# Kernel optimization log

Hardware: AMD Instinct MI355X
Metric: run time of the kernel (lower is better)

The kernel has to match this reference:

```python
import jax, jax.numpy as jnp
import numpy as np

PATCH_LEN = 16
PATCH_STRIDE = 8
DIM = 512
NUM_HEADS = 8
HEAD_DIM = DIM // NUM_HEADS
NUM_LAYERS = 4
MLP_HIDDEN = 4 * DIM
ROPE_BASE = 10000.0
LN_EPS = 1e-5


def setup_inputs() -> dict:
    key = jax.random.key(0)
    ks = jax.random.split(key, 20)
    B, T, C = 4, 8192, 7
    s = 0.02
    inp = {
        "x": jax.random.normal(ks[0], (B, T, C), dtype=jnp.float32),
        "W_emb": jax.random.normal(ks[1], (PATCH_LEN * C, DIM), dtype=jnp.float32) * s,
        "b_emb": jnp.zeros((DIM,), jnp.float32),
        "ln1_g": jnp.ones((NUM_LAYERS, DIM), jnp.float32),
        "ln1_b": jnp.zeros((NUM_LAYERS, DIM), jnp.float32),
        "W_qkv": jax.random.normal(ks[2], (NUM_LAYERS, DIM, 3 * DIM), dtype=jnp.float32) * s,
        "b_qkv": jnp.zeros((NUM_LAYERS, 3 * DIM), jnp.float32),
        "W_proj": jax.random.normal(ks[3], (NUM_LAYERS, DIM, DIM), dtype=jnp.float32) * s,
        "b_proj": jnp.zeros((NUM_LAYERS, DIM), jnp.float32),
        "ln2_g": jnp.ones((NUM_LAYERS, DIM), jnp.float32),
        "ln2_b": jnp.zeros((NUM_LAYERS, DIM), jnp.float32),
        "W_mlp1": jax.random.normal(ks[4], (NUM_LAYERS, DIM, MLP_HIDDEN), dtype=jnp.float32) * s,
        "b_mlp1": jnp.zeros((NUM_LAYERS, MLP_HIDDEN), jnp.float32),
        "W_mlp2": jax.random.normal(ks[5], (NUM_LAYERS, MLP_HIDDEN, DIM), dtype=jnp.float32) * s,
        "b_mlp2": jnp.zeros((NUM_LAYERS, DIM), jnp.float32),
        "lnf_g": jnp.ones((DIM,), jnp.float32),
        "lnf_b": jnp.zeros((DIM,), jnp.float32),
    }
    return inp


def _layer_norm(x, g, b):
    mu = jnp.mean(x, axis=-1, keepdims=True)
    var = jnp.mean(jnp.square(x - mu), axis=-1, keepdims=True)
    return (x - mu) * jax.lax.rsqrt(var + LN_EPS) * g + b


def _rotate_half(x):
    x1, x2 = jnp.split(x, 2, axis=-1)
    return jnp.concatenate((-x2, x1), axis=-1)


def _rope_cos_sin(seq_len):
    t = jnp.arange(seq_len, dtype=jnp.float32)
    inv_freq = 1.0 / (ROPE_BASE ** (jnp.arange(0, HEAD_DIM, 2, dtype=jnp.float32) / HEAD_DIM))
    freqs = jnp.outer(t, inv_freq)                      # [L, hd/2]
    emb = jnp.concatenate((freqs, freqs), axis=-1)      # [L, hd]
    return jnp.cos(emb), jnp.sin(emb)


def _forward(x, W_emb, b_emb, ln1_g, ln1_b, W_qkv, b_qkv, W_proj, b_proj,
             ln2_g, ln2_b, W_mlp1, b_mlp1, W_mlp2, b_mlp2, lnf_g, lnf_b):
    B, T, C = x.shape
    n = (T - PATCH_LEN) // PATCH_STRIDE + 1
    # torch unfold: [B, n, C, patch_len], then flattened as (C, patch_len)
    idx = jnp.arange(n)[:, None] * PATCH_STRIDE + jnp.arange(PATCH_LEN)[None, :]  # [n, P]
    patches = x[:, idx, :]                              # [B, n, P, C]
    patches = patches.transpose(0, 1, 3, 2).reshape(B, n, C * PATCH_LEN)
    emb = patches @ W_emb + b_emb                       # [B, n, D]

    cos, sin = _rope_cos_sin(n)                         # [n, hd]
    cos = cos[None, None, :, :]
    sin = sin[None, None, :, :]
    scale = HEAD_DIM ** -0.5

    h = emb
    for i in range(NUM_LAYERS):
        # --- attention ---
        y = _layer_norm(h, ln1_g[i], ln1_b[i])
        qkv = (y @ W_qkv[i] + b_qkv[i]).reshape(B, n, 3, NUM_HEADS, HEAD_DIM)
        qkv = qkv.transpose(2, 0, 3, 1, 4)              # [3, B, H, n, hd]
        q, k, v = qkv[0], qkv[1], qkv[2]
        q = q * cos + _rotate_half(q) * sin
        k = k * cos + _rotate_half(k) * sin
        attn = jax.nn.softmax(jnp.einsum('bhqd,bhkd->bhqk', q, k) * scale, axis=-1)
        o = jnp.einsum('bhqk,bhkd->bhqd', attn, v)      # [B, H, n, hd]
        o = o.transpose(0, 2, 1, 3).reshape(B, n, DIM)
        h = h + (o @ W_proj[i] + b_proj[i])
        # --- mlp ---
        y = _layer_norm(h, ln2_g[i], ln2_b[i])
        y = jax.nn.gelu(y @ W_mlp1[i] + b_mlp1[i], approximate=False)
        h = h + (y @ W_mlp2[i] + b_mlp2[i])

    x_out = _layer_norm(h, lnf_g, lnf_b)
    return emb, x_out


def reference(x, W_emb, b_emb, ln1_g, ln1_b, W_qkv, b_qkv, W_proj, b_proj,
              ln2_g, ln2_b, W_mlp1, b_mlp1, W_mlp2, b_mlp2, lnf_g, lnf_b):
    return _forward(x, W_emb, b_emb, ln1_g, ln1_b, W_qkv, b_qkv, W_proj, b_proj,
                    ln2_g, ln2_b, W_mlp1, b_mlp1, W_mlp2, b_mlp2, lnf_g, lnf_b)
```

## Files before the change

kernel.cpp:

```cpp
#include <hip/hip_runtime.h>
#include <hip/hip_bf16.h>
#include <math.h>

#define B_SZ 4
#define T_LEN 8192
#define C_IN 7
#define NPATCH 1023
#define DIM 512
#define NH 8
#define HD 64
#define NLAYERS 4
#define MLP_HID 2048
#define M_ROWS (B_SZ * NPATCH)
#define KEMB 128
#define LN_EPS 1e-5f

typedef __attribute__((ext_vector_type(8))) short short8;
typedef __attribute__((ext_vector_type(4))) float float4v;

static __device__ __forceinline__ unsigned short f2bf(float f) {
  __hip_bfloat16 h = __float2bfloat16(f);
  return *reinterpret_cast<unsigned short*>(&h);
}
static __device__ __forceinline__ float bf2f(unsigned short u) {
  return __uint_as_float(((unsigned)u) << 16);
}

__global__ __launch_bounds__(256) void patch_kernel(
    const float* __restrict__ x, unsigned short* __restrict__ Pm) {
  int idx = blockIdx.x * 256 + threadIdx.x;
  if (idx >= M_ROWS * KEMB) return;
  int row = idx >> 7, c = idx & 127;
  float v = 0.f;
  if (c < 112) {
    int b = row / NPATCH, i = row - b * NPATCH;
    int ci = c >> 4, p = c & 15;
    v = x[((size_t)b * T_LEN + (size_t)i * 8 + p) * C_IN + ci];
  }
  Pm[idx] = f2bf(v);
}

__global__ __launch_bounds__(256) void wemb_cvt_kernel(
    const float* __restrict__ W, unsigned short* __restrict__ Wt) {
  int idx = blockIdx.x * 256 + threadIdx.x;
  if (idx >= DIM * KEMB) return;
  int n = idx >> 7, k = idx & 127;
  float v = (k < 112) ? W[(size_t)k * DIM + n] : 0.f;
  Wt[idx] = f2bf(v);
}

template <bool BF>
__global__ __launch_bounds__(256) void ln_kernel(
    const float* __restrict__ in, const float* __restrict__ g,
    const float* __restrict__ bb, void* __restrict__ outv, int M) {
  int row = blockIdx.x * 4 + (threadIdx.x >> 6);
  if (row >= M) return;
  int lane = threadIdx.x & 63;
  const float* xr = in + (size_t)row * DIM;
  float v[8];
  float s = 0.f;
  #pragma unroll
  for (int k = 0; k < 8; ++k) { v[k] = xr[lane + 64 * k]; s += v[k]; }
  #pragma unroll
  for (int off = 32; off; off >>= 1) s += __shfl_down(s, off);
  s = __shfl(s, 0);
  float mu = s * (1.f / DIM);
  float q = 0.f;
  #pragma unroll
  for (int k = 0; k < 8; ++k) { float d = v[k] - mu; q = fmaf(d, d, q); }
  #pragma unroll
  for (int off = 32; off; off >>= 1) q += __shfl_down(q, off);
  q = __shfl(q, 0);
  float rstd = rsqrtf(q * (1.f / DIM) + LN_EPS);
  #pragma unroll
  for (int k = 0; k < 8; ++k) {
    int d = lane + 64 * k;
    float r = (v[k] - mu) * rstd * g[d] + bb[d];
    if (BF)
      ((unsigned short*)outv)[(size_t)row * DIM + d] = f2bf(r);
    else
      ((float*)outv)[(size_t)row * DIM + d] = r;
  }
}

__global__ __launch_bounds__(256) void wcvt_kernel(
    const float* __restrict__ W, unsigned short* __restrict__ Wt, int K, int N) {
  __shared__ float tile[32][33];
  int n0 = blockIdx.x * 32, k0 = blockIdx.y * 32, L = blockIdx.z;
  const float* Ws = W + (size_t)L * K * N;
  unsigned short* Wd = Wt + (size_t)L * K * N;
  int tx = threadIdx.x & 31, ty = threadIdx.x >> 5;
  #pragma unroll
  for (int i = 0; i < 4; ++i)
    tile[ty + i * 8][tx] = Ws[(size_t)(k0 + ty + i * 8) * N + n0 + tx];
  __syncthreads();
  #pragma unroll
  for (int i = 0; i < 4; ++i)
    Wd[(size_t)(n0 + ty + i * 8) * K + k0 + tx] = f2bf(tile[tx][ty + i * 8]);
}

__global__ __launch_bounds__(256) void rope_tab_kernel(float2* __restrict__ tab) {
  int idx = blockIdx.x * 256 + threadIdx.x;
  if (idx >= NPATCH * 32) return;
  int i = idx >> 5, j = idx & 31;
  float inv = powf(10000.0f, -(float)j * (1.0f / 32.0f));
  float sn, cs;
  sincosf((float)i * inv, &sn, &cs);
  tab[idx] = make_float2(cs, sn);
}

template <int TM, int TN, int EPI>
__global__ __launch_bounds__(256) void mfma_gemm(
    const unsigned short* __restrict__ A, const unsigned short* __restrict__ Bt,
    const float* __restrict__ bias, const float* __restrict__ res,
    float* __restrict__ Cf, float* __restrict__ Cf2,
    unsigned short* __restrict__ Cb, const float2* __restrict__ rtab,
    int M, int N, int K) {
  constexpr int WM = TM / 2, WN = TN / 2;
  constexpr int NI = WM / 16, NJ = WN / 16;
  constexpr int ACH = TM * 4;
  constexpr int TCH = (TM + TN) * 4;
  constexpr int CH = TCH / 256;
  __shared__ __align__(16) unsigned short As[2][TM][40];
  __shared__ __align__(16) unsigned short Bs[2][TN][40];
  const int bm = blockIdx.y * TM;
  const int bn = blockIdx.x * TN;
  const int tid = threadIdx.x;
  const int lane = tid & 63, wave = tid >> 6;
  const int quad = lane >> 4, l16 = lane & 15;
  const int wm = (wave & 1) * WM;
  const int wn = (wave >> 1) * WN;

  float4v acc[NI][NJ];
  #pragma unroll
  for (int i = 0; i < NI; ++i)
    #pragma unroll
    for (int j = 0; j < NJ; ++j)
      acc[i][j] = (float4v){0.f, 0.f, 0.f, 0.f};

  uint4 pr[CH];
  auto load_regs = [&](int kk) {
    #pragma unroll
    for (int it = 0; it < CH; ++it) {
      int c = tid + it * 256;
      if (c < ACH) {
        int row = c >> 2, ch = (c & 3) * 8;
        int gm = bm + row;
        pr[it] = make_uint4(0u, 0u, 0u, 0u);
        if (gm < M) pr[it] = *(const uint4*)(A + (size_t)gm * K + kk + ch);
      } else {
        int c2 = c - ACH;
        int row = c2 >> 2, ch = (c2 & 3) * 8;
        pr[it] = *(const uint4*)(Bt + (size_t)(bn + row) * K + kk + ch);
      }
    }
  };

  load_regs(0);
  int buf = 0;
  for (int k0 = 0; k0 < K; k0 += 32, buf ^= 1) {
    #pragma unroll
    for (int it = 0; it < CH; ++it) {
      int c = tid + it * 256;
      if (c < ACH)
        *(uint4*)&As[buf][c >> 2][(c & 3) * 8] = pr[it];
      else {
        int c2 = c - ACH;
        *(uint4*)&Bs[buf][c2 >> 2][(c2 & 3) * 8] = pr[it];
      }
    }
    if (k0 + 32 < K) load_regs(k0 + 32);
    __syncthreads();
    short8 af[NI], bfr[NJ];
    #pragma unroll
    for (int i = 0; i < NI; ++i)
      af[i] = *(const short8*)&As[buf][wm + i * 16 + l16][quad * 8];
    #pragma unroll
    for (int j = 0; j < NJ; ++j)
      bfr[j] = *(const short8*)&Bs[buf][wn + j * 16 + l16][quad * 8];
    #pragma unroll
    for (int i = 0; i < NI; ++i)
      #pragma unroll
      for (int j = 0; j < NJ; ++j)
        acc[i][j] = __builtin_amdgcn_mfma_f32_16x16x32_bf16(
            af[i], bfr[j], acc[i][j], 0, 0, 0);
  }

  if (EPI == 6) {
    const int sec = (bn + wn) >> 9;
    #pragma unroll
    for (int i = 0; i < NI; ++i) {
      int gm0 = bm + wm + i * 16 + quad * 4;
      #pragma unroll
      for (int r = 0; r < 4; ++r) {
        int gm = gm0 + r;
        if (gm >= M) continue;
        size_t rowoff = (size_t)gm * N;
        if (sec < 2) {
          int ip = gm; if (ip >= 2046) ip -= 2046; if (ip >= 1023) ip -= 1023;
          float sc = (sec == 0) ? 0.125f : 1.f;
          #pragma unroll
          for (int j = 0; j < 2; ++j) {
            int gn = bn + wn + j * 16 + l16;
            float v0 = acc[i][j][r] + bias[gn];
            float v1 = acc[i][j + 2][r] + bias[gn + 32];
            float2 t = rtab[ip * 32 + j * 16 + l16];
            Cb[rowoff + gn]      = f2bf((v0 * t.x - v1 * t.y) * sc);
            Cb[rowoff + gn + 32] = f2bf((v1 * t.x + v0 * t.y) * sc);
          }
        } else {
          #pragma unroll
          for (int j = 0; j < 4; ++j) {
            int gn = bn + wn + j * 16 + l16;
            Cb[rowoff + gn] = f2bf(acc[i][j][r] + bias[gn]);
          }
        }
      }
    }
    return;
  }

  #pragma unroll
  for (int j = 0; j < NJ; ++j) {
    int gn = bn + wn + j * 16 + l16;
    float bv = bias[gn];
    #pragma unroll
    for (int i = 0; i < NI; ++i) {
      int gm0 = bm + wm + i * 16 + quad * 4;
      #pragma unroll
      for (int r = 0; r < 4; ++r) {
        int gm = gm0 + r;
        if (gm < M) {
          float v = acc[i][j][r] + bv;
          size_t off = (size_t)gm * N + gn;
          if (EPI == 1) {
            Cf[off] = v + res[off];
          } else if (EPI == 2) {
            Cb[off] = f2bf(0.5f * v * (1.f + erff(v * 0.70710678118f)));
          } else if (EPI == 3) {
            Cb[off] = f2bf(v);
          } else {
            Cf[off] = v;
            Cf2[off] = v;
          }
        }
      }
    }
  }
}

#define APITCH 72

__global__ __launch_bounds__(256) void attn_kernel(
    const unsigned short* __restrict__ qkvb, unsigned short* __restrict__ o) {
  const int qt0 = blockIdx.x * 64;
  const int h = blockIdx.y;
  const int b = blockIdx.z;
  const int tid = threadIdx.x;
  const int lane = tid & 63, wave = tid >> 6;
  const int quad = lane >> 4, l16 = lane & 15;

  __shared__ __align__(16) unsigned short Qs[64][APITCH];
  __shared__ __align__(16) unsigned short Vt[2][HD][APITCH];
  __shared__ __align__(16) unsigned short Ps[4][16][APITCH];

  const int sr = tid >> 2;
  const int sc0 = (tid & 3) * 16;
  {
    int qi = qt0 + sr;
    uint4 a = make_uint4(0u, 0u, 0u, 0u), b2 = a;
    if (qi < NPATCH) {
      const uint4* src = (const uint4*)(qkvb + (size_t)(b * NPATCH + qi) * (3 * DIM) + h * HD + sc0);
      a = src[0]; b2 = src[1];
    }
    *(uint4*)&Qs[sr][sc0] = a;
    *(uint4*)&Qs[sr][sc0 + 8] = b2;
  }

  const int kp = tid & 31, dg = tid >> 5;
  uint4 pv0, pv1;
  auto load_v = [&](int j0) {
    pv0 = pv1 = make_uint4(0u, 0u, 0u, 0u);
    int j = j0 + 2 * kp;
    const unsigned short* vb = qkvb + (size_t)(b * NPATCH + j) * (3 * DIM) + 2 * DIM + h * HD + dg * 8;
    if (j < NPATCH)     pv0 = *(const uint4*)vb;
    if (j + 1 < NPATCH) pv1 = *(const uint4*)(vb + 3 * DIM);
  };

  const unsigned short* kbase = qkvb + (size_t)b * NPATCH * (3 * DIM) + DIM + (size_t)h * HD;
  uint4 nk0[4], nk1[4];
  auto load_k = [&](int j0) {
    #pragma unroll
    for (int j = 0; j < 4; ++j) {
      int row = j0 + j * 16 + l16;
      nk0[j] = make_uint4(0u, 0u, 0u, 0u);
      nk1[j] = nk0[j];
      if (row < NPATCH) {
        const uint4* kr = (const uint4*)(kbase + (size_t)row * (3 * DIM) + quad * 8);
        nk0[j] = kr[0];
        nk1[j] = kr[4];
      }
    }
  };

  load_v(0);
  load_k(0);
  __syncthreads();

  short8 aq0 = *(const short8*)&Qs[wave * 16 + l16][quad * 8];
  short8 aq1 = *(const short8*)&Qs[wave * 16 + l16][32 + quad * 8];

  float4v accO[4];
  #pragma unroll
  for (int j2 = 0; j2 < 4; ++j2) accO[j2] = (float4v){0.f, 0.f, 0.f, 0.f};
  float m_run[4] = {-1e30f, -1e30f, -1e30f, -1e30f};
  float lp[4] = {0.f, 0.f, 0.f, 0.f};

  int buf = 0;
  for (int j0 = 0; j0 < NPATCH; j0 += 64, buf ^= 1) {
    {
      unsigned short va[8], vb8[8];
      *(uint4*)&va[0] = pv0;
      *(uint4*)&vb8[0] = pv1;
      #pragma unroll
      for (int u = 0; u < 8; ++u) {
        unsigned pk = (unsigned)va[u] | ((unsigned)vb8[u] << 16);
        *(unsigned*)&Vt[buf][dg * 8 + u][2 * kp] = pk;
      }
    }
    __syncthreads();

    float4v s[4];
    __builtin_amdgcn_s_setprio(1);
    #pragma unroll
    for (int j = 0; j < 4; ++j) {
      s[j] = (float4v){0.f, 0.f, 0.f, 0.f};
      s[j] = __builtin_amdgcn_mfma_f32_16x16x32_bf16(
          aq0, __builtin_bit_cast(short8, nk0[j]), s[j], 0, 0, 0);
      s[j] = __builtin_amdgcn_mfma_f32_16x16x32_bf16(
          aq1, __builtin_bit_cast(short8, nk1[j]), s[j], 0, 0, 0);
    }
    __builtin_amdgcn_s_setprio(0);

    if (j0 + 64 < NPATCH) { load_k(j0 + 64); load_v(j0 + 64); }

    float mx[4];
    #pragma unroll
    for (int r = 0; r < 4; ++r)
      mx[r] = fmaxf(fmaxf(s[0][r], s[1][r]), fmaxf(s[2][r], s[3][r]));
    #pragma unroll
    for (int mask = 1; mask < 16; mask <<= 1)
      #pragma unroll
      for (int r = 0; r < 4; ++r)
        mx[r] = fmaxf(mx[r], __shfl_xor(mx[r], mask));
    float g = fmaxf(fmaxf(mx[0] - m_run[0], mx[1] - m_run[1]),
                    fmaxf(mx[2] - m_run[2], mx[3] - m_run[3]));
    if (!__all(g <= 8.f)) {
      #pragma unroll
      for (int r = 0; r < 4; ++r) {
        float mnew = fmaxf(m_run[r], mx[r]);
        float al = __expf(m_run[r] - mnew);
        m_run[r] = mnew;
        lp[r] *= al;
        #pragma unroll
        for (int j2 = 0; j2 < 4; ++j2) accO[j2][r] *= al;
      }
    }
    #pragma unroll
    for (int j = 0; j < 4; ++j) {
      bool valid = (j0 + j * 16 + l16) < NPATCH;
      #pragma unroll
      for (int r = 0; r < 4; ++r) {
        float p = valid ? __expf(s[j][r] - m_run[r]) : 0.f;
        lp[r] += p;
        Ps[wave][quad * 4 + r][j * 16 + l16] = f2bf(p);
      }
    }

    short8 pa0 = *(const short8*)&Ps[wave][l16][quad * 8];
    short8 pa1 = *(const short8*)&Ps[wave][l16][32 + quad * 8];
    __builtin_amdgcn_s_setprio(1);
    #pragma unroll
    for (int j2 = 0; j2 < 4; ++j2) {
      short8 v0 = *(const short8*)&Vt[buf][j2 * 16 + l16][quad * 8];
      short8 v1 = *(const short8*)&Vt[buf][j2 * 16 + l16][32 + quad * 8];
      accO[j2] = __builtin_amdgcn_mfma_f32_16x16x32_bf16(pa0, v0, accO[j2], 0, 0, 0);
      accO[j2] = __builtin_amdgcn_mfma_f32_16x16x32_bf16(pa1, v1, accO[j2], 0, 0, 0);
    }
    __builtin_amdgcn_s_setprio(0);
  }

  #pragma unroll
  for (int mask = 1; mask < 16; mask <<= 1)
    #pragma unroll
    for (int r = 0; r < 4; ++r)
      lp[r] += __shfl_xor(lp[r], mask);

  #pragma unroll
  for (int r = 0; r < 4; ++r) {
    int qi = qt0 + wave * 16 + quad * 4 + r;
    if (qi < NPATCH) {
      float inv = 1.f / lp[r];
      size_t off = (size_t)(b * NPATCH + qi) * DIM + h * HD + l16;
      #pragma unroll
      for (int j2 = 0; j2 < 4; ++j2)
        o[off + j2 * 16] = f2bf(accO[j2][r] * inv);
    }
  }
}

extern "C" void kernel_launch(void* const* d_in, const int* in_sizes, int n_in,
                              void* d_out, int out_size, void* d_ws, size_t ws_size,
                              hipStream_t stream) {
  const float* x      = (const float*)d_in[0];
  const float* W_emb  = (const float*)d_in[1];
  const float* b_emb  = (const float*)d_in[2];
  const float* ln1_g  = (const float*)d_in[3];
  const float* ln1_b  = (const float*)d_in[4];
  const float* W_qkv  = (const float*)d_in[5];
  const float* b_qkv  = (const float*)d_in[6];
  const float* W_proj = (const float*)d_in[7];
  const float* b_proj = (const float*)d_in[8];
  const float* ln2_g  = (const float*)d_in[9];
  const float* ln2_b  = (const float*)d_in[10];
  const float* W_mlp1 = (const float*)d_in[11];
  const float* b_mlp1 = (const float*)d_in[12];
  const float* W_mlp2 = (const float*)d_in[13];
  const float* b_mlp2 = (const float*)d_in[14];
  const float* lnf_g  = (const float*)d_in[15];
  const float* lnf_b  = (const float*)d_in[16];
  float* out = (float*)d_out;

  float* h              = (float*)d_ws;
  unsigned short* qkvb  = (unsigned short*)(h + (size_t)M_ROWS * DIM);
  unsigned short* midbf = qkvb;
  unsigned short* ybf   = qkvb + (size_t)M_ROWS * MLP_HID;
  unsigned short* obf   = ybf;
  unsigned short* wqkv_t  = ybf + (size_t)M_ROWS * DIM;
  unsigned short* wproj_t = wqkv_t  + (size_t)NLAYERS * DIM * 3 * DIM;
  unsigned short* wmlp1_t = wproj_t + (size_t)NLAYERS * DIM * DIM;
  unsigned short* wmlp2_t = wmlp1_t + (size_t)NLAYERS * DIM * MLP_HID;
  float2* rtab = (float2*)(wmlp2_t + (size_t)NLAYERS * MLP_HID * DIM);
  unsigned short* Pm    = (unsigned short*)(rtab + (size_t)NPATCH * 32);
  unsigned short* Wembt = Pm + (size_t)M_ROWS * KEMB;

  wcvt_kernel<<<dim3(3 * DIM / 32, DIM / 32, NLAYERS), 256, 0, stream>>>(W_qkv,  wqkv_t,  DIM, 3 * DIM);
  wcvt_kernel<<<dim3(DIM / 32, DIM / 32, NLAYERS),     256, 0, stream>>>(W_proj, wproj_t, DIM, DIM);
  wcvt_kernel<<<dim3(MLP_HID / 32, DIM / 32, NLAYERS), 256, 0, stream>>>(W_mlp1, wmlp1_t, DIM, MLP_HID);
  wcvt_kernel<<<dim3(DIM / 32, MLP_HID / 32, NLAYERS), 256, 0, stream>>>(W_mlp2, wmlp2_t, MLP_HID, DIM);
  rope_tab_kernel<<<(NPATCH * 32 + 255) / 256, 256, 0, stream>>>(rtab);
  patch_kernel<<<(M_ROWS * KEMB + 255) / 256, 256, 0, stream>>>(x, Pm);
  wemb_cvt_kernel<<<(DIM * KEMB + 255) / 256, 256, 0, stream>>>(W_emb, Wembt);

  const int MT64 = (M_ROWS + 63) / 64;
  const int LNG = (M_ROWS + 3) / 4;

  mfma_gemm<64, 64, 5><<<dim3(DIM / 64, MT64), 256, 0, stream>>>(
      Pm, Wembt, b_emb, nullptr, out, h, nullptr, nullptr, M_ROWS, DIM, KEMB);

  for (int L = 0; L < NLAYERS; ++L) {
    ln_kernel<true><<<LNG, 256, 0, stream>>>(h, ln1_g + L * DIM, ln1_b + L * DIM, ybf, M_ROWS);
    mfma_gemm<64, 128, 6><<<dim3(3 * DIM / 128, MT64), 256, 0, stream>>>(
        ybf, wqkv_t + (size_t)L * DIM * 3 * DIM, b_qkv + L * 3 * DIM,
        nullptr, nullptr, nullptr, qkvb, rtab, M_ROWS, 3 * DIM, DIM);
    attn_kernel<<<dim3((NPATCH + 63) / 64, NH, B_SZ), 256, 0, stream>>>(qkvb, obf);
    mfma_gemm<64, 64, 1><<<dim3(DIM / 64, MT64), 256, 0, stream>>>(
        obf, wproj_t + (size_t)L * DIM * DIM, b_proj + L * DIM,
        h, h, nullptr, nullptr, nullptr, M_ROWS, DIM, DIM);
    ln_kernel<true><<<LNG, 256, 0, stream>>>(h, ln2_g + L * DIM, ln2_b + L * DIM, ybf, M_ROWS);
    mfma_gemm<64, 128, 2><<<dim3(MLP_HID / 128, MT64), 256, 0, stream>>>(
        ybf, wmlp1_t + (size_t)L * DIM * MLP_HID, b_mlp1 + L * MLP_HID,
        nullptr, nullptr, nullptr, midbf, nullptr, M_ROWS, MLP_HID, DIM);
    mfma_gemm<64, 64, 1><<<dim3(DIM / 64, MT64), 256, 0, stream>>>(
        midbf, wmlp2_t + (size_t)L * MLP_HID * DIM, b_mlp2 + L * DIM,
        h, h, nullptr, nullptr, nullptr, M_ROWS, DIM, MLP_HID);
  }

  ln_kernel<false><<<LNG, 256, 0, stream>>>(h, lnf_g, lnf_b, out + (size_t)M_ROWS * DIM, M_ROWS);
}
```

Measured before the change: 712.4 us.

## Split attention over key dimension with separate combine kernel

Attention now splits the key range into two chunks, so the grid doubles from 512 to 1024 blocks. Block IDs are remapped so that blocks sharing a (batch, chunk, head) group land on the same XCD. Each block writes unnormalized fp32 partial outputs plus running max and sum, and a new combine kernel merges the two halves and writes bf16. Q is now loaded directly into registers instead of going through shared memory. The aim is better CU occupancy on the many-CU GPU, paid for with extra global traffic for the fp32 partials and one more kernel launch per layer.

```diff
diff --git a/kernel.cpp b/kernel.cpp
--- a/kernel.cpp
+++ b/kernel.cpp
@@ -14,6 +14,8 @@
 #define M_ROWS (B_SZ * NPATCH)
 #define KEMB 128
 #define LN_EPS 1e-5f
+#define NSPLIT 2
+#define KCHUNK 512
 
 typedef __attribute__((ext_vector_type(8))) short short8;
 typedef __attribute__((ext_vector_type(4))) float float4v;
@@ -252,29 +254,33 @@
 #define APITCH 72
 
 __global__ __launch_bounds__(256) void attn_kernel(
-    const unsigned short* __restrict__ qkvb, unsigned short* __restrict__ o) {
-  const int qt0 = blockIdx.x * 64;
-  const int h = blockIdx.y;
-  const int b = blockIdx.z;
+    const unsigned short* __restrict__ qkvb,
+    float* __restrict__ Opart, float2* __restrict__ ml) {
+  const int bid = blockIdx.x;
+  const int xcd = bid & 7, slot = bid >> 3;
+  const int qt = slot & 15, ghi = slot >> 4;
+  const int g = ghi * 8 + xcd;
+  const int h = g & 7;
+  const int z = g >> 3;
+  const int b = z >> 1, c = z & 1;
+  const int qt0 = qt * 64;
+  const int j0base = c * KCHUNK;
+
   const int tid = threadIdx.x;
   const int lane = tid & 63, wave = tid >> 6;
   const int quad = lane >> 4, l16 = lane & 15;
 
-  __shared__ __align__(16) unsigned short Qs[64][APITCH];
   __shared__ __align__(16) unsigned short Vt[2][HD][APITCH];
   __shared__ __align__(16) unsigned short Ps[4][16][APITCH];
 
-  const int sr = tid >> 2;
-  const int sc0 = (tid & 3) * 16;
+  short8 aq0 = {0, 0, 0, 0, 0, 0, 0, 0}, aq1 = aq0;
   {
-    int qi = qt0 + sr;
-    uint4 a = make_uint4(0u, 0u, 0u, 0u), b2 = a;
-    if (qi < NPATCH) {
-      const uint4* src = (const uint4*)(qkvb + (size_t)(b * NPATCH + qi) * (3 * DIM) + h * HD + sc0);
-      a = src[0]; b2 = src[1];
-    }
-    *(uint4*)&Qs[sr][sc0] = a;
-    *(uint4*)&Qs[sr][sc0 + 8] = b2;
+    int qrow = qt0 + wave * 16 + l16;
+    if (qrow < NPATCH) {
+      const uint4* qr = (const uint4*)(qkvb + (size_t)(b * NPATCH + qrow) * (3 * DIM) + h * HD + quad * 8);
+      aq0 = __builtin_bit_cast(short8, qr[0]);
+      aq1 = __builtin_bit_cast(short8, qr[4]);
+    }
   }
 
   const int kp = tid & 31, dg = tid >> 5;
@@ -303,12 +309,8 @@
     }
   };
 
-  load_v(0);
-  load_k(0);
-  __syncthreads();
-
-  short8 aq0 = *(const short8*)&Qs[wave * 16 + l16][quad * 8];
-  short8 aq1 = *(const short8*)&Qs[wave * 16 + l16][32 + quad * 8];
+  load_v(j0base);
+  load_k(j0base);
 
   float4v accO[4];
   #pragma unroll
@@ -317,7 +319,8 @@
   float lp[4] = {0.f, 0.f, 0.f, 0.f};
 
   int buf = 0;
-  for (int j0 = 0; j0 < NPATCH; j0 += 64, buf ^= 1) {
+  for (int t = 0; t < KCHUNK / 64; ++t, buf ^= 1) {
+    const int j0 = j0base + t * 64;
     {
       unsigned short va[8], vb8[8];
       *(uint4*)&va[0] = pv0;
@@ -342,7 +345,7 @@
     }
     __builtin_amdgcn_s_setprio(0);
 
-    if (j0 + 64 < NPATCH) { load_k(j0 + 64); load_v(j0 + 64); }
+    if (t + 1 < KCHUNK / 64) { load_k(j0 + 64); load_v(j0 + 64); }
 
     float mx[4];
     #pragma unroll
@@ -353,9 +356,9 @@
       #pragma unroll
       for (int r = 0; r < 4; ++r)
         mx[r] = fmaxf(mx[r], __shfl_xor(mx[r], mask));
-    float g = fmaxf(fmaxf(mx[0] - m_run[0], mx[1] - m_run[1]),
-                    fmaxf(mx[2] - m_run[2], mx[3] - m_run[3]));
-    if (!__all(g <= 8.f)) {
+    float gmax = fmaxf(fmaxf(mx[0] - m_run[0], mx[1] - m_run[1]),
+                       fmaxf(mx[2] - m_run[2], mx[3] - m_run[3]));
+    if (!__all(gmax <= 8.f)) {
       #pragma unroll
       for (int r = 0; r < 4; ++r) {
         float mnew = fmaxf(m_run[r], mx[r]);
@@ -396,17 +399,39 @@
     for (int r = 0; r < 4; ++r)
       lp[r] += __shfl_xor(lp[r], mask);
 
+  const size_t cb = (((size_t)c * B_SZ + b) * NH + h) * NPATCH;
   #pragma unroll
   for (int r = 0; r < 4; ++r) {
     int qi = qt0 + wave * 16 + quad * 4 + r;
     if (qi < NPATCH) {
-      float inv = 1.f / lp[r];
-      size_t off = (size_t)(b * NPATCH + qi) * DIM + h * HD + l16;
+      size_t ro = (cb + qi) * HD + l16;
       #pragma unroll
       for (int j2 = 0; j2 < 4; ++j2)
-        o[off + j2 * 16] = f2bf(accO[j2][r] * inv);
-    }
-  }
+        Opart[ro + j2 * 16] = accO[j2][r];
+      if (l16 == 0) ml[cb + qi] = make_float2(m_run[r], lp[r]);
+    }
+  }
+}
+
+__global__ __launch_bounds__(256) void attn_combine(
+    const float* __restrict__ Opart, const float2* __restrict__ ml,
+    unsigned short* __restrict__ o) {
+  int idx = blockIdx.x * 256 + threadIdx.x;
+  if (idx >= B_SZ * NH * NPATCH * HD) return;
+  int d = idx & 63;
+  int rhi = idx >> 6;
+  const size_t half = (size_t)B_SZ * NH * NPATCH;
+  float2 m0 = ml[rhi], m1 = ml[half + rhi];
+  float ms = fmaxf(m0.x, m1.x);
+  float w0 = __expf(m0.x - ms), w1 = __expf(m1.x - ms);
+  float lst = w0 * m0.y + w1 * m1.y;
+  float a0 = Opart[(size_t)rhi * HD + d];
+  float a1 = Opart[half * HD + (size_t)rhi * HD + d];
+  float val = (w0 * a0 + w1 * a1) / lst;
+  int qi = rhi % NPATCH;
+  int bh = rhi / NPATCH;
+  int hh = bh & 7, bb = bh >> 3;
+  o[((size_t)bb * NPATCH + qi) * DIM + hh * HD + d] = f2bf(val);
 }
 
 extern "C" void kernel_launch(void* const* d_in, const int* in_sizes, int n_in,
@@ -443,6 +468,8 @@
   float2* rtab = (float2*)(wmlp2_t + (size_t)NLAYERS * MLP_HID * DIM);
   unsigned short* Pm    = (unsigned short*)(rtab + (size_t)NPATCH * 32);
   unsigned short* Wembt = Pm + (size_t)M_ROWS * KEMB;
+  float* Opart          = (float*)(Wembt + (size_t)DIM * KEMB);
+  float2* mlbuf         = (float2*)(Opart + (size_t)NSPLIT * B_SZ * NH * NPATCH * HD);
 
   wcvt_kernel<<<dim3(3 * DIM / 32, DIM / 32, NLAYERS), 256, 0, stream>>>(W_qkv,  wqkv_t,  DIM, 3 * DIM);
   wcvt_kernel<<<dim3(DIM / 32, DIM / 32, NLAYERS),     256, 0, stream>>>(W_proj, wproj_t, DIM, DIM);
@@ -454,6 +481,7 @@
 
   const int MT64 = (M_ROWS + 63) / 64;
   const int LNG = (M_ROWS + 3) / 4;
+  const int CMB = (B_SZ * NH * NPATCH * HD + 255) / 256;
 
   mfma_gemm<64, 64, 5><<<dim3(DIM / 64, MT64), 256, 0, stream>>>(
       Pm, Wembt, b_emb, nullptr, out, h, nullptr, nullptr, M_ROWS, DIM, KEMB);
@@ -463,7 +491,8 @@
     mfma_gemm<64, 128, 6><<<dim3(3 * DIM / 128, MT64), 256, 0, stream>>>(
         ybf, wqkv_t + (size_t)L * DIM * 3 * DIM, b_qkv + L * 3 * DIM,
         nullptr, nullptr, nullptr, qkvb, rtab, M_ROWS, 3 * DIM, DIM);
-    attn_kernel<<<dim3((NPATCH + 63) / 64, NH, B_SZ), 256, 0, stream>>>(qkvb, obf);
+    attn_kernel<<<dim3(16 * 8 * B_SZ * NSPLIT), 256, 0, stream>>>(qkvb, Opart, mlbuf);
+    attn_combine<<<CMB, 256, 0, stream>>>(Opart, mlbuf, obf);
     mfma_gemm<64, 64, 1><<<dim3(DIM / 64, MT64), 256, 0, stream>>>(
         obf, wproj_t + (size_t)L * DIM * DIM, b_proj + L * DIM,
         h, h, nullptr, nullptr, nullptr, M_ROWS, DIM, DIM);
```

Measured after the change: 765.0 us. 7.4% more time.
